# Kernel tuning notes

Hardware: AMD Instinct MI355X
Metric: run time of the kernel (lower is better)

## Reference

```python
import jax, jax.numpy as jnp
import numpy as np

N, E, H, NF, MN, ME = 4096, 65536, 128, 4, 8, 4
DEPTH, RATIO, NT = 5, 0.2, 2


def _k_list():
    ks, n = [], N
    for _ in range(DEPTH):
        n = int(np.ceil(RATIO * n))
        ks.append(n)
    return ks

K_LIST = _k_list()  # [820, 164, 33, 7, 2]


def _gcn(A, x, W, b, fill):
    # GCNConv on dense adjacency: D^-1/2 (A + fill*I) D^-1/2 @ (x W) + b
    n = A.shape[0]
    Ah = A + fill * jnp.eye(n, dtype=A.dtype)
    deg = jnp.sum(Ah, axis=1)
    dinv = jnp.where(deg > 0, jax.lax.rsqrt(jnp.maximum(deg, 1e-12)), 0.0)
    return (dinv[:, None] * Ah * dinv[None, :]) @ (x @ W) + b


def _augment(A):
    # GraphUNet.augment_adj: remove self loops, add weight-1 loops, A@A, remove self loops
    n = A.shape[0]
    eye = jnp.eye(n, dtype=A.dtype)
    A1 = A * (1.0 - eye) + eye
    A2 = A1 @ A1
    return A2 * (1.0 - eye)


def _topk_pool(A, x, w, k):
    # TopKPooling: score = tanh(x.w / ||w||), keep top-k, scale kept features by score
    score = jnp.tanh((x @ w) / jnp.linalg.norm(w))
    sv, perm = jax.lax.top_k(score, k)
    return x[perm] * sv[:, None], A[perm][:, perm], perm


def _graph_unet(A0, x, Wd0, bd0, Wd, bd, pool_w, Wu, bu):
    act = jax.nn.relu
    x = act(_gcn(A0, x, Wd0, bd0, 2.0))  # improved GCN: fill=2
    xs, As, perms = [x], [A0], []
    A = A0
    for i in range(DEPTH):
        A = _augment(A)
        x, A, perm = _topk_pool(A, x, pool_w[i], K_LIST[i])
        x = act(_gcn(A, x, Wd[i], bd[i], 2.0))
        if i < DEPTH - 1:
            xs.append(x)
            As.append(A)
        perms.append(perm)
    for i in range(DEPTH):
        j = DEPTH - 1 - i
        res, Aj, perm = xs[j], As[j], perms[j]
        up = jnp.zeros_like(res).at[perm].set(x)
        x = _gcn(Aj, res + up, Wu[i], bu[i], 2.0)  # sum_res=True
        if i < DEPTH - 1:
            x = act(x)
    return x


def _forward(F_0, mesh_node, mesh_edge, Wm, bm, Wd0, bd0, Wd, bd, pool_w,
             Wu, bu, Wout, bout, edge_index, n_time):
    src, dst = edge_index[0], edge_index[1]
    A = jnp.zeros((N, N), jnp.float32).at[dst, src].add(1.0)  # dst aggregates from src
    h = jnp.zeros((N, H), jnp.float32)
    F_cur = F_0
    Fs = []
    for _ in range(n_time):
        node_attr = jnp.concatenate([F_cur, mesh_node, h], axis=1)
        # Input: per-edge cat([x_i, x_j, e]) -> Linear -> scatter-sum by dst
        msg = jnp.concatenate([node_attr[dst], node_attr[src], mesh_edge], axis=1) @ Wm + bm
        h1 = jax.nn.relu(jax.ops.segment_sum(msg, dst, num_segments=N))
        h2 = _graph_unet(A, h1, Wd0, bd0, Wd, bd, pool_w, Wu, bu)
        h = jax.lax.stop_gradient(h2)
        h2 = jax.nn.relu(h2)
        F_next = _gcn(A, jnp.concatenate([h1, h2], axis=1), Wout, bout, 1.0)
        Fs.append(F_next)
        F_cur = jax.lax.stop_gradient(F_next)
    return jnp.stack(Fs, axis=1)  # [N, n_time, NF]


def setup_inputs() -> dict:
    key = jax.random.key(0)
    ks = jax.random.split(key, 12)
    s = 0.05
    node_in = NF + MN + H
    return {
        "F_0": jax.random.normal(ks[0], (N, NF), jnp.float32),
        "mesh_node": jax.random.normal(ks[1], (N, MN), jnp.float32),
        "mesh_edge": jax.random.normal(ks[2], (E, ME), jnp.float32),
        "Wm": jax.random.normal(ks[3], (2 * node_in + ME, H), jnp.float32) * s,
        "bm": jnp.zeros((H,), jnp.float32),
        "Wd0": jax.random.normal(ks[4], (H, H), jnp.float32) * s,
        "bd0": jnp.zeros((H,), jnp.float32),
        "Wd": jax.random.normal(ks[5], (DEPTH, H, H), jnp.float32) * s,
        "bd": jnp.zeros((DEPTH, H), jnp.float32),
        "pool_w": jax.random.normal(ks[6], (DEPTH, H), jnp.float32) * s,
        "Wu": jax.random.normal(ks[7], (DEPTH, H, H), jnp.float32) * s,
        "bu": jnp.zeros((DEPTH, H), jnp.float32),
        "Wout": jax.random.normal(ks[8], (2 * H, NF), jnp.float32) * s,
        "bout": jnp.zeros((NF,), jnp.float32),
        "edge_index": jax.random.randint(ks[9], (2, E), 0, N, dtype=jnp.int32),
        "n_time": NT,
    }


def reference(F_0, mesh_node, mesh_edge, Wm, bm, Wd0, bd0, Wd, bd, pool_w,
              Wu, bu, Wout, bout, edge_index, n_time):
    return _forward(F_0, mesh_node, mesh_edge, Wm, bm, Wd0, bd0, Wd, bd,
                    pool_w, Wu, bu, Wout, bout, edge_index, n_time)
```

## Files before the change

kernel.cpp:

```cpp
#include <hip/hip_runtime.h>
#include <math.h>

#define NN 4096
#define EE 65536
#define H 128
#define NF 4
#define MNODE 8
#define MEDGE 4
#define NT 2

__global__ void k_count(const int* __restrict__ dst, int* __restrict__ cnt) {
  int e = blockIdx.x * 256 + threadIdx.x;
  if (e < EE) atomicAdd(&cnt[dst[e]], 1);
}

__global__ void k_scan(const int* __restrict__ cnt, int* __restrict__ rp) {
  __shared__ int sh[1024];
  int t = threadIdx.x;
  int v0 = cnt[4*t], v1 = cnt[4*t+1], v2 = cnt[4*t+2], v3 = cnt[4*t+3];
  int p1 = v0, p2 = v0 + v1, p3 = p2 + v2, tot = p3 + v3;
  sh[t] = tot; __syncthreads();
  for (int off = 1; off < 1024; off <<= 1) {
    int add = (t >= off) ? sh[t-off] : 0;
    __syncthreads();
    sh[t] += add;
    __syncthreads();
  }
  int base = sh[t] - tot;
  rp[4*t] = base; rp[4*t+1] = base + p1; rp[4*t+2] = base + p2; rp[4*t+3] = base + p3;
  if (t == 1023) rp[NN] = sh[t];
}

__global__ void k_fill(const int* __restrict__ ei, int* __restrict__ cursor, int* __restrict__ cols) {
  int e = blockIdx.x * 256 + threadIdx.x;
  if (e < EE) {
    int d = ei[EE + e], s = ei[e];
    int pos = atomicAdd(&cursor[d], 1);
    cols[pos] = s;
  }
}

__global__ void k_dinv0(const int* __restrict__ cnt, float* __restrict__ d2, float* __restrict__ d1) {
  int i = blockIdx.x * 256 + threadIdx.x;
  if (i < NN) {
    float c = (float)cnt[i];
    d2[i] = 1.f / sqrtf(c + 2.f);
    d1[i] = 1.f / sqrtf(c + 1.f);
  }
}

__global__ void k_pwnorm(const float* __restrict__ pw, float* __restrict__ pwn) {
  int l = blockIdx.x, t = threadIdx.x;
  float a = pw[l*H + t], b = pw[l*H + 64 + t];
  float s = a*a + b*b;
  for (int off = 32; off > 0; off >>= 1) s += __shfl_down(s, off);
  if (t == 0) pwn[l] = sqrtf(s);
}

__global__ void k_segS(const int* __restrict__ dst, const float* __restrict__ me, float* __restrict__ S) {
  int e = blockIdx.x * 256 + threadIdx.x;
  if (e < EE) {
    int d = dst[e];
#pragma unroll
    for (int m = 0; m < MEDGE; m++) atomicAdd(&S[d*MEDGE + m], me[e*MEDGE + m]);
  }
}

__device__ __forceinline__ void score_epilogue(float v, int row, int t,
                                               const float* pw, const float* pwn1,
                                               float* scoreo, unsigned long long* keyso,
                                               int* ranko, float* r2) {
  float sp = v * pw[t];
  for (int off = 32; off > 0; off >>= 1) sp += __shfl_down(sp, off);
  if ((t & 63) == 0) r2[t >> 6] = sp;
  __syncthreads();
  if (t == 0) {
    float s = r2[0] + r2[1];
    float sc = tanhf(s / pwn1[0]);
    scoreo[row] = sc;
    float s2 = sc + 0.0f;
    unsigned u = __float_as_uint(s2);
    u ^= (unsigned)(((int)u >> 31)) | 0x80000000u;
    keyso[row] = ((unsigned long long)u << 12) | (unsigned)(4095 - row);
    ranko[row] = 0;
  }
}

__global__ void k_mm_cat(const float* __restrict__ F, const float* __restrict__ mn,
                         const float* __restrict__ h, const float* __restrict__ Wm,
                         float* __restrict__ P, float* __restrict__ Q) {
  __shared__ float as[140];
  int row = blockIdx.x, t = threadIdx.x;
  for (int c = t; c < 140; c += 128) {
    float v;
    if (c < NF) v = F[row*NF + c];
    else if (c < NF + MNODE) v = mn[row*MNODE + (c - NF)];
    else v = h[(size_t)row*H + (c - NF - MNODE)];
    as[c] = v;
  }
  __syncthreads();
  const float* BQ = Wm + 140*H;
  float ap = 0.f, aq = 0.f;
  for (int kk = 0; kk < 140; kk++) {
    float a = as[kk];
    ap += a * Wm[kk*H + t];
    aq += a * BQ[kk*H + t];
  }
  P[(size_t)row*H + t] = ap;
  Q[(size_t)row*H + t] = aq;
}

__global__ void k_spmm_h1_mm(const float* __restrict__ Q, const int* __restrict__ rp,
                             const int* __restrict__ cols, const float* __restrict__ Pm,
                             const float* __restrict__ bm, const float* __restrict__ S,
                             const float* __restrict__ WmB, const int* __restrict__ cnt,
                             const float* __restrict__ Wd0, const float* __restrict__ dinv2,
                             float* __restrict__ h1, float* __restrict__ tsb) {
  __shared__ float hs[128];
  int i = blockIdx.x, t = threadIdx.x;
  float acc = 0.f;
  int beg = rp[i], end = rp[i+1];
  for (int e = beg; e < end; e++) acc += Q[(size_t)cols[e]*H + t];
  float v = (float)cnt[i] * (Pm[(size_t)i*H + t] + bm[t]) + acc;
#pragma unroll
  for (int m = 0; m < MEDGE; m++) v += S[i*MEDGE + m] * WmB[m*H + t];
  v = fmaxf(v, 0.f);
  h1[(size_t)i*H + t] = v;
  hs[t] = v;
  __syncthreads();
  float a2 = 0.f;
  for (int kk = 0; kk < H; kk++) a2 += hs[kk] * Wd0[kk*H + t];
  tsb[(size_t)i*H + t] = a2 * dinv2[i];
}

__global__ void k_spmm_fused(const float* __restrict__ ts, const int* __restrict__ rp,
                             const int* __restrict__ cols, const float* __restrict__ dinv,
                             float fill, const float* __restrict__ bias, int relu,
                             float* __restrict__ out,
                             const float* __restrict__ pw, const float* __restrict__ pwn1,
                             float* __restrict__ scoreo, unsigned long long* __restrict__ keyso,
                             int* __restrict__ ranko) {
  __shared__ float r2[2];
  int i = blockIdx.x, t = threadIdx.x;
  float acc = 0.f;
  int beg = rp[i], end = rp[i+1];
  for (int e = beg; e < end; e++) acc += ts[(size_t)cols[e]*H + t];
  float v;
  if (dinv) {
    v = dinv[i] * (acc + fill * ts[(size_t)i*H + t]) + bias[t];
    if (relu) v = fmaxf(v, 0.f);
  } else v = acc;
  out[(size_t)i*H + t] = v;
  if (pw) score_epilogue(v, i, t, pw, pwn1, scoreo, keyso, ranko, r2);
}

__global__ void k_count_rank(const unsigned long long* __restrict__ keys, int n,
                             int* __restrict__ rank) {
  __shared__ unsigned long long sk[256];
  int t = threadIdx.x;
  int j = blockIdx.y * 256 + t;
  sk[t] = (j < n) ? keys[j] : 0ull;
  __syncthreads();
  int i = blockIdx.x * 256 + t;
  if (i >= n) return;
  unsigned long long ki = keys[i];
  int r = 0;
#pragma unroll 8
  for (int jj = 0; jj < 256; jj++) r += (sk[jj] > ki) ? 1 : 0;
  if (r) atomicAdd(&rank[i], r);
}

__global__ void k_select(const float* __restrict__ score, const int* __restrict__ rank,
                         int n, int k, int* __restrict__ perm, float* __restrict__ sv,
                         int* __restrict__ inv) {
  int i = blockIdx.x * 256 + threadIdx.x;
  if (i < n) {
    int r = rank[i];
    inv[i] = r;
    if (r < k) { perm[r] = i; sv[r] = score[i]; }
  }
}

__global__ void k_rank820(const float* __restrict__ score, const unsigned long long* __restrict__ keys,
                          int n, int k, int* __restrict__ perm, float* __restrict__ sv,
                          int* __restrict__ inv) {
  __shared__ unsigned long long ks[832];
  int t = threadIdx.x;
  for (int i = t; i < n; i += 1024) ks[i] = keys[i];
  __syncthreads();
  if (t < n) {
    unsigned long long ki = ks[t];
    int r = 0;
    for (int j = 0; j < n; j++) r += (ks[j] > ki) ? 1 : 0;
    inv[t] = r;
    if (r < k) { perm[r] = t; sv[r] = score[t]; }
  }
}

__global__ void k_mm_pool(const float* __restrict__ x, const int* __restrict__ perm,
                          const float* __restrict__ sv, const float* __restrict__ B,
                          float* __restrict__ C, const float* __restrict__ dinv) {
  __shared__ float as[128];
  int row = blockIdx.x, t = threadIdx.x;
  as[t] = x[(size_t)perm[row]*H + t] * sv[row];
  __syncthreads();
  float acc = 0.f;
  for (int kk = 0; kk < H; kk++) acc += as[kk] * B[kk*H + t];
  C[(size_t)row*H + t] = acc * dinv[row];
}

__global__ void k_mm_rb(const float* __restrict__ A, const float* __restrict__ B,
                        float* __restrict__ C, const float* __restrict__ dinv) {
  __shared__ float as[128];
  int row = blockIdx.x, t = threadIdx.x;
  as[t] = A[(size_t)row*H + t];
  __syncthreads();
  float acc = 0.f;
  for (int kk = 0; kk < H; kk++) acc += as[kk] * B[kk*H + t];
  C[(size_t)row*H + t] = acc * dinv[row];
}

__global__ void k_pool_small(const float* __restrict__ score, const unsigned long long* __restrict__ keys,
                             const float* __restrict__ x, int n, int k,
                             int* __restrict__ perm, float* __restrict__ sv,
                             int* __restrict__ inv, float* __restrict__ xp) {
  __shared__ unsigned long long ks[256];
  __shared__ int permS[40];
  __shared__ float svS[40];
  int t = threadIdx.x;
  ks[t] = (t < n) ? keys[t] : 0ull;
  __syncthreads();
  if (t < n) {
    unsigned long long ki = ks[t];
    int r = 0;
    for (int j = 0; j < n; j++) r += (ks[j] > ki) ? 1 : 0;
    inv[t] = r;
    if (r < k) {
      float sc = score[t];
      permS[r] = t; svS[r] = sc;
      perm[r] = t; sv[r] = sc;
    }
  }
  __syncthreads();
  for (int idx = t; idx < k*H; idx += 256) {
    int r = idx >> 7, c = idx & 127;
    xp[idx] = x[(size_t)permS[r]*H + c] * svS[r];
  }
}

__global__ void k_a820_f(const int* __restrict__ rp, const int* __restrict__ cols,
                         const int* __restrict__ perm, float* __restrict__ A820,
                         float* __restrict__ dv) {
  __shared__ float acc[NN];
  __shared__ float red[256];
  int r = blockIdx.x, t = threadIdx.x;
  for (int i = t; i < NN; i += 256) acc[i] = 0.f;
  __syncthreads();
  int pi = perm[r];
  int beg = rp[pi], end = rp[pi+1];
  for (int e = beg + t; e < end; e += 256) { int c = cols[e]; if (c != pi) atomicAdd(&acc[c], 1.f); }
  if (t == 0) atomicAdd(&acc[pi], 1.f);
  int wv = t >> 6, ln = t & 63;
  for (int e0 = beg + wv; e0 < end; e0 += 4) {
    int c = cols[e0];
    if (c == pi) continue;
    int b2 = rp[c], e2 = rp[c+1];
    for (int e = b2 + ln; e < e2; e += 64) { int c2 = cols[e]; if (c2 != c) atomicAdd(&acc[c2], 1.f); }
    if (ln == 0) atomicAdd(&acc[c], 1.f);
  }
  __syncthreads();
  float local = 0.f;
  for (int cc = t; cc < 820; cc += 256) {
    float val = (cc == r) ? 0.f : acc[perm[cc]];
    A820[(size_t)r*820 + cc] = val;
    local += val;
  }
  red[t] = local; __syncthreads();
  for (int off = 128; off > 0; off >>= 1) { if (t < off) red[t] += red[t+off]; __syncthreads(); }
  if (t == 0) dv[r] = 1.f / sqrtf(red[0] + 2.f);
}

__global__ void k_gathercols(const float* __restrict__ A, int n, const int* __restrict__ perm,
                             int knext, float* __restrict__ AP) {
  int idx = blockIdx.x * 256 + threadIdx.x;
  int total = n * knext;
  if (idx >= total) return;
  int kk = idx / knext, c = idx - kk * knext;
  AP[idx] = A[(size_t)kk * n + perm[c]];
}

__global__ void k_augpool2_f(const float* __restrict__ A, const float* __restrict__ AP,
                             int n, const int* __restrict__ perm, int knext,
                             float* __restrict__ out, float* __restrict__ dv) {
  __shared__ float rowb[832];
  __shared__ float red[256];
  int r = blockIdx.x, t = threadIdx.x;
  int pr = perm[r];
  for (int i = t; i < n; i += 256) rowb[i] = A[(size_t)pr*n + i];
  __syncthreads();
  float local = 0.f;
  for (int c = t; c < knext; c += 256) {
    float dot = 0.f;
#pragma unroll 8
    for (int kk = 0; kk < n; kk++) dot += rowb[kk] * AP[(size_t)kk*knext + c];
    float val = (c == r) ? 0.f : (dot + 2.f * AP[(size_t)pr*knext + c]);
    out[(size_t)r*knext + c] = val;
    local += val;
  }
  red[t] = local; __syncthreads();
  for (int off = 128; off > 0; off >>= 1) { if (t < off) red[t] += red[t+off]; __syncthreads(); }
  if (t == 0) dv[r] = 1.f / sqrtf(red[0] + 2.f);
}

__global__ void k_augpool_small(const float* __restrict__ A, int n, const int* __restrict__ perm,
                                int knext, float* __restrict__ out, float* __restrict__ dv) {
  __shared__ float rowb[256];
  __shared__ float rsum;
  int r = blockIdx.x, t = threadIdx.x;
  int pr = perm[r];
  if (t < n) rowb[t] = A[(size_t)pr*n + t];
  if (t == 0) rsum = 0.f;
  __syncthreads();
  int g = t >> 3, lane = t & 7;
  for (int c = g; c < knext; c += 32) {
    int pc = perm[c];
    float part = 0.f;
    for (int kk = lane; kk < n; kk += 8) part += rowb[kk] * A[(size_t)kk*n + pc];
    part += __shfl_down(part, 4, 8);
    part += __shfl_down(part, 2, 8);
    part += __shfl_down(part, 1, 8);
    if (lane == 0) {
      float val = (c == r) ? 0.f : (part + 2.f * rowb[pc]);
      out[(size_t)r*knext + c] = val;
      atomicAdd(&rsum, val);
    }
  }
  __syncthreads();
  if (t == 0) dv[r] = 1.f / sqrtf(rsum + 2.f);
}

__global__ void k_dense_gcn(const float* __restrict__ A, int n, const float* __restrict__ ts,
                            const float* __restrict__ dinv, float fill, const float* __restrict__ bias,
                            int relu, float* __restrict__ out,
                            const float* __restrict__ pw, const float* __restrict__ pwn1,
                            float* __restrict__ scoreo, unsigned long long* __restrict__ keyso,
                            int* __restrict__ ranko) {
  __shared__ float r2[2];
  int i = blockIdx.x, t = threadIdx.x;
  const float* Ar = A + (size_t)i * n;
  float acc = 0.f;
  int kk = 0;
  int n4 = n & ~3;
#pragma unroll 2
  for (; kk < n4; kk += 4) {
    float a0 = Ar[kk+0], a1 = Ar[kk+1], a2 = Ar[kk+2], a3 = Ar[kk+3];
    float t0 = ts[(size_t)(kk+0)*H + t];
    float t1 = ts[(size_t)(kk+1)*H + t];
    float t2 = ts[(size_t)(kk+2)*H + t];
    float t3 = ts[(size_t)(kk+3)*H + t];
    acc += a0*t0; acc += a1*t1; acc += a2*t2; acc += a3*t3;
  }
  for (; kk < n; kk++) acc += Ar[kk] * ts[(size_t)kk*H + t];
  float v = dinv[i] * (acc + fill * ts[(size_t)i*H + t]) + bias[t];
  if (relu) v = fmaxf(v, 0.f);
  out[(size_t)i*H + t] = v;
  if (pw) score_epilogue(v, i, t, pw, pwn1, scoreo, keyso, ranko, r2);
}

__global__ void k_upproj(const float* __restrict__ xs, const int* __restrict__ inv,
                         const float* __restrict__ xcur, int kk,
                         const float* __restrict__ W, const float* __restrict__ dinv,
                         float* __restrict__ tsb) {
  __shared__ float hs[128];
  int i = blockIdx.x, t = threadIdx.x;
  int r = inv[i];
  float v = xs[(size_t)i*H + t];
  if (r < kk) v += xcur[(size_t)r*H + t];
  hs[t] = v;
  __syncthreads();
  float acc = 0.f;
  for (int k2 = 0; k2 < H; k2++) acc += hs[k2] * W[k2*H + t];
  tsb[(size_t)i*H + t] = acc * dinv[i];
}

__global__ void k_outproj_r(const float* __restrict__ h1, const float* __restrict__ hbuf,
                            const float* __restrict__ Wout, const float* __restrict__ dinv1,
                            float* __restrict__ ts2) {
  int row = blockIdx.x, t = threadIdx.x;
  float p0 = 0.f, p1 = 0.f, p2 = 0.f, p3 = 0.f;
#pragma unroll
  for (int half = 0; half < 2; half++) {
    float a = h1[(size_t)row*H + half*64 + t];
    const float* w = Wout + (half*64 + t)*4;
    p0 += a*w[0]; p1 += a*w[1]; p2 += a*w[2]; p3 += a*w[3];
    float b = fmaxf(hbuf[(size_t)row*H + half*64 + t], 0.f);
    const float* w2 = Wout + (128 + half*64 + t)*4;
    p0 += b*w2[0]; p1 += b*w2[1]; p2 += b*w2[2]; p3 += b*w2[3];
  }
  for (int off = 32; off > 0; off >>= 1) {
    p0 += __shfl_down(p0, off); p1 += __shfl_down(p1, off);
    p2 += __shfl_down(p2, off); p3 += __shfl_down(p3, off);
  }
  if (t == 0) {
    float d = dinv1[row];
    ts2[row*4+0] = d*p0; ts2[row*4+1] = d*p1; ts2[row*4+2] = d*p2; ts2[row*4+3] = d*p3;
  }
}

__global__ void k_gcn_out(const float* __restrict__ ts2, const int* __restrict__ rp,
                          const int* __restrict__ cols, const float* __restrict__ dinv1,
                          const float* __restrict__ bout, float* __restrict__ Fcur,
                          float* __restrict__ dout, int tstep) {
  int i = blockIdx.x, t = threadIdx.x;
  int f = t & 3;
  float acc = 0.f;
  int beg = rp[i], end = rp[i+1];
  for (int e = beg + (t >> 2); e < end; e += 16) acc += ts2[cols[e]*4 + f];
  for (int off = 32; off >= 4; off >>= 1) acc += __shfl_down(acc, off);
  if (t < 4) {
    float v = dinv1[i] * (acc + ts2[i*4 + f]) + bout[f];
    Fcur[i*4 + f] = v;
    dout[i*(NT*NF) + tstep*NF + f] = v;
  }
}

extern "C" void kernel_launch(void* const* d_in, const int* in_sizes, int n_in,
                              void* d_out, int out_size, void* d_ws, size_t ws_size,
                              hipStream_t stream) {
  const float* F0        = (const float*)d_in[0];
  const float* mesh_node = (const float*)d_in[1];
  const float* mesh_edge = (const float*)d_in[2];
  const float* Wm        = (const float*)d_in[3];
  const float* bm        = (const float*)d_in[4];
  const float* Wd0       = (const float*)d_in[5];
  const float* bd0       = (const float*)d_in[6];
  const float* Wd        = (const float*)d_in[7];
  const float* bd        = (const float*)d_in[8];
  const float* pool_w    = (const float*)d_in[9];
  const float* Wu        = (const float*)d_in[10];
  const float* bu        = (const float*)d_in[11];
  const float* Wout      = (const float*)d_in[12];
  const float* bout      = (const float*)d_in[13];
  const int*   ei        = (const int*)d_in[14];
  float* out = (float*)d_out;

  char* p = (char*)d_ws;
  auto carve = [&](size_t bytes) -> char* {
    char* r = p;
    p += (bytes + 255) & ~(size_t)255;
    return r;
  };
  int*   cnt    = (int*)carve((size_t)NN*4);
  int*   rp     = (int*)carve((size_t)(NN+1)*4);
  int*   cursor = (int*)carve((size_t)NN*4);
  int*   cols   = (int*)carve((size_t)EE*4);
  int*   permb  = (int*)carve((size_t)5*832*4);
  float* svb    = (float*)carve((size_t)5*832*4);
  float* dinv2  = (float*)carve((size_t)NN*4);
  float* dinv1  = (float*)carve((size_t)NN*4);
  float* pwn    = (float*)carve(8*4);
  float* S      = (float*)carve((size_t)NN*MEDGE*4);
  int*   invb   = (int*)carve((size_t)5*NN*4);
  float* P      = (float*)carve((size_t)NN*H*4);
  float* Q      = (float*)carve((size_t)NN*H*4);
  float* h1     = (float*)carve((size_t)NN*H*4);
  float* hbuf   = (float*)carve((size_t)NN*H*4);
  float* tsb    = (float*)carve((size_t)NN*H*4);
  float* tmp    = (float*)carve((size_t)NN*H*4);
  float* x0     = (float*)carve((size_t)NN*H*4);
  float* x1     = (float*)carve((size_t)820*H*4);
  float* x2     = (float*)carve((size_t)164*H*4);
  float* x3     = (float*)carve((size_t)33*H*4);
  float* x4     = (float*)carve((size_t)7*H*4);
  float* xp     = (float*)carve((size_t)820*H*4);
  float* xcur   = (float*)carve((size_t)820*H*4);
  float* score  = (float*)carve((size_t)NN*4);
  unsigned long long* keysb = (unsigned long long*)carve((size_t)NN*8);
  int*   rankb  = (int*)carve((size_t)NN*4);
  float* A820   = (float*)carve((size_t)820*820*4);
  float* A164   = (float*)carve((size_t)164*164*4);
  float* A33    = (float*)carve((size_t)33*33*4);
  float* A7     = (float*)carve((size_t)7*7*4);
  float* A2b    = (float*)carve((size_t)2*2*4);
  float* dv820  = (float*)carve(820*4);
  float* dv164  = (float*)carve(164*4);
  float* dv33   = (float*)carve(33*4);
  float* dv7    = (float*)carve(7*4);
  float* dv2    = (float*)carve(2*4);
  float* ts2    = (float*)carve((size_t)NN*NF*4);
  float* Fcur   = (float*)carve((size_t)NN*NF*4);

  float* AP = tmp;

  int* perml[5]; float* svl[5]; int* invl[5];
  for (int l = 0; l < 5; l++) {
    perml[l] = permb + l*832; svl[l] = svb + l*832; invl[l] = invb + l*NN;
  }

  hipMemsetAsync(cnt, 0, (size_t)NN*4, stream);
  hipMemsetAsync(S, 0, (size_t)NN*MEDGE*4, stream);
  hipMemsetAsync(hbuf, 0, (size_t)NN*H*4, stream);
  k_count<<<EE/256, 256, 0, stream>>>(ei + EE, cnt);
  k_scan<<<1, 1024, 0, stream>>>(cnt, rp);
  hipMemcpyAsync(cursor, rp, (size_t)NN*4, hipMemcpyDeviceToDevice, stream);
  k_fill<<<EE/256, 256, 0, stream>>>(ei, cursor, cols);
  k_dinv0<<<NN/256, 256, 0, stream>>>(cnt, dinv2, dinv1);
  k_pwnorm<<<5, 64, 0, stream>>>(pool_w, pwn);
  k_segS<<<EE/256, 256, 0, stream>>>(ei + EE, mesh_edge, S);
  hipMemcpyAsync(Fcur, F0, (size_t)NN*NF*4, hipMemcpyDeviceToDevice, stream);

  for (int step = 0; step < NT; step++) {
    k_mm_cat<<<NN, 128, 0, stream>>>(Fcur, mesh_node, hbuf, Wm, P, Q);
    k_spmm_h1_mm<<<NN, 128, 0, stream>>>(Q, rp, cols, P, bm, S, Wm + 280*H, cnt,
                                         Wd0, dinv2, h1, tsb);
    k_spmm_fused<<<NN, 128, 0, stream>>>(tsb, rp, cols, dinv2, 2.f, bd0, 1, x0,
                                         pool_w, pwn, score, keysb, rankb);

    k_count_rank<<<dim3(16, 16), 256, 0, stream>>>(keysb, NN, rankb);
    k_select<<<16, 256, 0, stream>>>(score, rankb, NN, 820, perml[0], svl[0], invl[0]);
    k_a820_f<<<820, 256, 0, stream>>>(rp, cols, perml[0], A820, dv820);
    k_mm_pool<<<820, 128, 0, stream>>>(x0, perml[0], svl[0], Wd, tsb, dv820);
    k_dense_gcn<<<820, 128, 0, stream>>>(A820, 820, tsb, dv820, 2.f, bd, 1, x1,
                                         pool_w + H, pwn + 1, score, keysb, rankb);

    k_rank820<<<1, 1024, 0, stream>>>(score, keysb, 820, 164, perml[1], svl[1], invl[1]);
    k_gathercols<<<(820*164 + 255)/256, 256, 0, stream>>>(A820, 820, perml[1], 164, AP);
    k_augpool2_f<<<164, 256, 0, stream>>>(A820, AP, 820, perml[1], 164, A164, dv164);
    k_mm_pool<<<164, 128, 0, stream>>>(x1, perml[1], svl[1], Wd + 1*H*H, tsb, dv164);
    k_dense_gcn<<<164, 128, 0, stream>>>(A164, 164, tsb, dv164, 2.f, bd + 1*H, 1, x2,
                                         pool_w + 2*H, pwn + 2, score, keysb, rankb);

    k_pool_small<<<1, 256, 0, stream>>>(score, keysb, x2, 164, 33, perml[2], svl[2], invl[2], xp);
    k_augpool_small<<<33, 256, 0, stream>>>(A164, 164, perml[2], 33, A33, dv33);
    k_mm_rb<<<33, 128, 0, stream>>>(xp, Wd + 2*H*H, tsb, dv33);
    k_dense_gcn<<<33, 128, 0, stream>>>(A33, 33, tsb, dv33, 2.f, bd + 2*H, 1, x3,
                                        pool_w + 3*H, pwn + 3, score, keysb, rankb);

    k_pool_small<<<1, 256, 0, stream>>>(score, keysb, x3, 33, 7, perml[3], svl[3], invl[3], xp);
    k_augpool_small<<<7, 256, 0, stream>>>(A33, 33, perml[3], 7, A7, dv7);
    k_mm_rb<<<7, 128, 0, stream>>>(xp, Wd + 3*H*H, tsb, dv7);
    k_dense_gcn<<<7, 128, 0, stream>>>(A7, 7, tsb, dv7, 2.f, bd + 3*H, 1, x4,
                                       pool_w + 4*H, pwn + 4, score, keysb, rankb);

    k_pool_small<<<1, 256, 0, stream>>>(score, keysb, x4, 7, 2, perml[4], svl[4], invl[4], xp);
    k_augpool_small<<<2, 256, 0, stream>>>(A7, 7, perml[4], 2, A2b, dv2);
    k_mm_rb<<<2, 128, 0, stream>>>(xp, Wd + 4*H*H, tsb, dv2);
    k_dense_gcn<<<2, 128, 0, stream>>>(A2b, 2, tsb, dv2, 2.f, bd + 4*H, 1, xcur,
                                       nullptr, nullptr, nullptr, nullptr, nullptr);

    k_upproj<<<7, 128, 0, stream>>>(x4, invl[4], xcur, 2, Wu, dv7, tsb);
    k_dense_gcn<<<7, 128, 0, stream>>>(A7, 7, tsb, dv7, 2.f, bu, 1, xcur,
                                       nullptr, nullptr, nullptr, nullptr, nullptr);
    k_upproj<<<33, 128, 0, stream>>>(x3, invl[3], xcur, 7, Wu + 1*H*H, dv33, tsb);
    k_dense_gcn<<<33, 128, 0, stream>>>(A33, 33, tsb, dv33, 2.f, bu + 1*H, 1, xcur,
                                        nullptr, nullptr, nullptr, nullptr, nullptr);
    k_upproj<<<164, 128, 0, stream>>>(x2, invl[2], xcur, 33, Wu + 2*H*H, dv164, tsb);
    k_dense_gcn<<<164, 128, 0, stream>>>(A164, 164, tsb, dv164, 2.f, bu + 2*H, 1, xcur,
                                         nullptr, nullptr, nullptr, nullptr, nullptr);
    k_upproj<<<820, 128, 0, stream>>>(x1, invl[1], xcur, 164, Wu + 3*H*H, dv820, tsb);
    k_dense_gcn<<<820, 128, 0, stream>>>(A820, 820, tsb, dv820, 2.f, bu + 3*H, 1, xcur,
                                         nullptr, nullptr, nullptr, nullptr, nullptr);
    k_upproj<<<NN, 128, 0, stream>>>(x0, invl[0], xcur, 820, Wu + 4*H*H, dinv2, tsb);
    k_spmm_fused<<<NN, 128, 0, stream>>>(tsb, rp, cols, dinv2, 2.f, bu + 4*H, 0, hbuf,
                                         nullptr, nullptr, nullptr, nullptr, nullptr);

    k_outproj_r<<<NN, 64, 0, stream>>>(h1, hbuf, Wout, dinv1, ts2);
    k_gcn_out<<<NN, 64, 0, stream>>>(ts2, rp, cols, dinv1, bout, Fcur, out, step);
  }
}
```

Baseline: 764.0 us.

## Fuse deepest pooling levels and first two up-steps into one single-block kernel

```diff
diff --git a/kernel.cpp b/kernel.cpp
--- a/kernel.cpp
+++ b/kernel.cpp
@@ -381,6 +381,189 @@
   float acc = 0.f;
   for (int k2 = 0; k2 < H; k2++) acc += hs[k2] * W[k2*H + t];
   tsb[(size_t)i*H + t] = acc * dinv[i];
+}
+
+__global__ __launch_bounds__(256) void k_deep2(
+    const float* __restrict__ x3g, const float* __restrict__ A33g,
+    const float* __restrict__ dv33g, const float* __restrict__ score,
+    const unsigned long long* __restrict__ keys,
+    const float* __restrict__ pool_w, const float* __restrict__ pwn,
+    const float* __restrict__ Wd, const float* __restrict__ bd,
+    const float* __restrict__ Wu, const float* __restrict__ bu,
+    float* __restrict__ xcur) {
+  __shared__ float x3s[33*128];
+  __shared__ float xpb[33*128];
+  __shared__ float tsbb[33*128];
+  __shared__ float x4s[7*128];
+  __shared__ float xc7[7*128];
+  __shared__ float xc2[2*128];
+  __shared__ float A33s[33*33];
+  __shared__ float A7s[49];
+  __shared__ float A2s[4];
+  __shared__ float dv33s[33], dv7s[7], dv2s[2];
+  __shared__ int   perm7[7], perm2[2], inv33s[33], inv7s[7];
+  __shared__ float sv7[7], sv2[2];
+  __shared__ unsigned long long ksh[33];
+  __shared__ float scs[33];
+  int t = threadIdx.x;
+
+  for (int i = t; i < 33*128; i += 256) x3s[i] = x3g[i];
+  for (int i = t; i < 33*33; i += 256) A33s[i] = A33g[i];
+  if (t < 33) { dv33s[t] = dv33g[t]; ksh[t] = keys[t]; scs[t] = score[t]; }
+  __syncthreads();
+
+  if (t < 33) {
+    unsigned long long ki = ksh[t];
+    int r = 0;
+    for (int j = 0; j < 33; j++) r += (ksh[j] > ki) ? 1 : 0;
+    inv33s[t] = r;
+    if (r < 7) { perm7[r] = t; sv7[r] = scs[t]; }
+  }
+  __syncthreads();
+  for (int o = t; o < 7*128; o += 256) {
+    int r = o >> 7, c = o & 127;
+    xpb[o] = x3s[perm7[r]*128 + c] * sv7[r];
+  }
+  if (t < 49) {
+    int r = t / 7, c = t - 7*r;
+    int pr = perm7[r], pc = perm7[c];
+    float dot = 0.f;
+    for (int kk = 0; kk < 33; kk++) dot += A33s[pr*33 + kk] * A33s[kk*33 + pc];
+    A7s[t] = (r == c) ? 0.f : (dot + 2.f * A33s[pr*33 + pc]);
+  }
+  __syncthreads();
+  if (t < 7) {
+    float s = 0.f;
+    for (int c = 0; c < 7; c++) s += A7s[t*7 + c];
+    dv7s[t] = 1.f / sqrtf(s + 2.f);
+  }
+  __syncthreads();
+  {
+    const float* Wd3 = Wd + 3*H*H;
+    for (int o = t; o < 7*128; o += 256) {
+      int r = o >> 7, c = o & 127;
+      float acc = 0.f;
+      for (int kk = 0; kk < H; kk++) acc += xpb[r*128 + kk] * Wd3[kk*H + c];
+      tsbb[o] = acc * dv7s[r];
+    }
+  }
+  __syncthreads();
+  {
+    const float* bd3 = bd + 3*H;
+    for (int o = t; o < 7*128; o += 256) {
+      int r = o >> 7, c = o & 127;
+      float acc = 0.f;
+      for (int kk = 0; kk < 7; kk++) acc += A7s[r*7 + kk] * tsbb[kk*128 + c];
+      float v = dv7s[r] * (acc + 2.f * tsbb[o]) + bd3[c];
+      x4s[o] = fmaxf(v, 0.f);
+    }
+  }
+  __syncthreads();
+  if (t < 7) {
+    const float* pw4 = pool_w + 4*H;
+    float s = 0.f;
+    for (int c = 0; c < H; c++) s += x4s[t*128 + c] * pw4[c];
+    float sc = tanhf(s / pwn[4]);
+    scs[t] = sc;
+    float s2 = sc + 0.0f;
+    unsigned u = __float_as_uint(s2);
+    u ^= (unsigned)(((int)u >> 31)) | 0x80000000u;
+    ksh[t] = ((unsigned long long)u << 12) | (unsigned)(4095 - t);
+  }
+  __syncthreads();
+  if (t < 7) {
+    unsigned long long ki = ksh[t];
+    int r = 0;
+    for (int j = 0; j < 7; j++) r += (ksh[j] > ki) ? 1 : 0;
+    inv7s[t] = r;
+    if (r < 2) { perm2[r] = t; sv2[r] = scs[t]; }
+  }
+  __syncthreads();
+  for (int o = t; o < 2*128; o += 256) {
+    int r = o >> 7, c = o & 127;
+    xpb[o] = x4s[perm2[r]*128 + c] * sv2[r];
+  }
+  if (t < 4) {
+    int r = t >> 1, c = t & 1;
+    int pr = perm2[r], pc = perm2[c];
+    float dot = 0.f;
+    for (int kk = 0; kk < 7; kk++) dot += A7s[pr*7 + kk] * A7s[kk*7 + pc];
+    A2s[t] = (r == c) ? 0.f : (dot + 2.f * A7s[pr*7 + pc]);
+  }
+  __syncthreads();
+  if (t < 2) dv2s[t] = 1.f / sqrtf(A2s[t*2] + A2s[t*2+1] + 2.f);
+  __syncthreads();
+  {
+    const float* Wd4 = Wd + 4*H*H;
+    for (int o = t; o < 2*128; o += 256) {
+      int r = o >> 7, c = o & 127;
+      float acc = 0.f;
+      for (int kk = 0; kk < H; kk++) acc += xpb[r*128 + kk] * Wd4[kk*H + c];
+      tsbb[o] = acc * dv2s[r];
+    }
+  }
+  __syncthreads();
+  {
+    const float* bd4 = bd + 4*H;
+    for (int o = t; o < 2*128; o += 256) {
+      int r = o >> 7, c = o & 127;
+      float acc = A2s[r*2 + 0] * tsbb[c] + A2s[r*2 + 1] * tsbb[128 + c];
+      float v = dv2s[r] * (acc + 2.f * tsbb[o]) + bd4[c];
+      xc2[o] = fmaxf(v, 0.f);
+    }
+  }
+  __syncthreads();
+  for (int o = t; o < 7*128; o += 256) {
+    int r = o >> 7, c = o & 127;
+    float v = x4s[o];
+    int rr = inv7s[r];
+    if (rr < 2) v += xc2[rr*128 + c];
+    xpb[o] = v;
+  }
+  __syncthreads();
+  for (int o = t; o < 7*128; o += 256) {
+    int r = o >> 7, c = o & 127;
+    float acc = 0.f;
+    for (int kk = 0; kk < H; kk++) acc += xpb[r*128 + kk] * Wu[kk*H + c];
+    tsbb[o] = acc * dv7s[r];
+  }
+  __syncthreads();
+  for (int o = t; o < 7*128; o += 256) {
+    int r = o >> 7, c = o & 127;
+    float acc = 0.f;
+    for (int kk = 0; kk < 7; kk++) acc += A7s[r*7 + kk] * tsbb[kk*128 + c];
+    float v = dv7s[r] * (acc + 2.f * tsbb[o]) + bu[c];
+    xc7[o] = fmaxf(v, 0.f);
+  }
+  __syncthreads();
+  for (int o = t; o < 33*128; o += 256) {
+    int r = o >> 7, c = o & 127;
+    float v = x3s[o];
+    int rr = inv33s[r];
+    if (rr < 7) v += xc7[rr*128 + c];
+    xpb[o] = v;
+  }
+  __syncthreads();
+  {
+    const float* Wu1 = Wu + 1*H*H;
+    for (int o = t; o < 33*128; o += 256) {
+      int r = o >> 7, c = o & 127;
+      float acc = 0.f;
+      for (int kk = 0; kk < H; kk++) acc += xpb[r*128 + kk] * Wu1[kk*H + c];
+      tsbb[o] = acc * dv33s[r];
+    }
+  }
+  __syncthreads();
+  {
+    const float* bu1 = bu + 1*H;
+    for (int o = t; o < 33*128; o += 256) {
+      int r = o >> 7, c = o & 127;
+      float acc = 0.f;
+      for (int kk = 0; kk < 33; kk++) acc += A33s[r*33 + kk] * tsbb[kk*128 + c];
+      float v = dv33s[r] * (acc + 2.f * tsbb[o]) + bu1[c];
+      xcur[o] = fmaxf(v, 0.f);
+    }
+  }
 }
 
 __global__ void k_outproj_r(const float* __restrict__ h1, const float* __restrict__ hbuf,
@@ -491,6 +674,7 @@
   float* Fcur   = (float*)carve((size_t)NN*NF*4);
 
   float* AP = tmp;
+  (void)x4; (void)xp; (void)A7; (void)A2b; (void)dv7; (void)dv2;
 
   int* perml[5]; float* svl[5]; int* invl[5];
   for (int l = 0; l < 5; l++) {
@@ -530,30 +714,15 @@
     k_dense_gcn<<<164, 128, 0, stream>>>(A164, 164, tsb, dv164, 2.f, bd + 1*H, 1, x2,
                                          pool_w + 2*H, pwn + 2, score, keysb, rankb);
 
-    k_pool_small<<<1, 256, 0, stream>>>(score, keysb, x2, 164, 33, perml[2], svl[2], invl[2], xp);
+    k_pool_small<<<1, 256, 0, stream>>>(score, keysb, x2, 164, 33, perml[2], svl[2], invl[2], tsb);
     k_augpool_small<<<33, 256, 0, stream>>>(A164, 164, perml[2], 33, A33, dv33);
-    k_mm_rb<<<33, 128, 0, stream>>>(xp, Wd + 2*H*H, tsb, dv33);
-    k_dense_gcn<<<33, 128, 0, stream>>>(A33, 33, tsb, dv33, 2.f, bd + 2*H, 1, x3,
+    k_mm_rb<<<33, 128, 0, stream>>>(tsb, Wd + 2*H*H, tmp, dv33);
+    k_dense_gcn<<<33, 128, 0, stream>>>(A33, 33, tmp, dv33, 2.f, bd + 2*H, 1, x3,
                                         pool_w + 3*H, pwn + 3, score, keysb, rankb);
 
-    k_pool_small<<<1, 256, 0, stream>>>(score, keysb, x3, 33, 7, perml[3], svl[3], invl[3], xp);
-    k_augpool_small<<<7, 256, 0, stream>>>(A33, 33, perml[3], 7, A7, dv7);
-    k_mm_rb<<<7, 128, 0, stream>>>(xp, Wd + 3*H*H, tsb, dv7);
-    k_dense_gcn<<<7, 128, 0, stream>>>(A7, 7, tsb, dv7, 2.f, bd + 3*H, 1, x4,
-                                       pool_w + 4*H, pwn + 4, score, keysb, rankb);
-
-    k_pool_small<<<1, 256, 0, stream>>>(score, keysb, x4, 7, 2, perml[4], svl[4], invl[4], xp);
-    k_augpool_small<<<2, 256, 0, stream>>>(A7, 7, perml[4], 2, A2b, dv2);
-    k_mm_rb<<<2, 128, 0, stream>>>(xp, Wd + 4*H*H, tsb, dv2);
-    k_dense_gcn<<<2, 128, 0, stream>>>(A2b, 2, tsb, dv2, 2.f, bd + 4*H, 1, xcur,
-                                       nullptr, nullptr, nullptr, nullptr, nullptr);
-
-    k_upproj<<<7, 128, 0, stream>>>(x4, invl[4], xcur, 2, Wu, dv7, tsb);
-    k_dense_gcn<<<7, 128, 0, stream>>>(A7, 7, tsb, dv7, 2.f, bu, 1, xcur,
-                                       nullptr, nullptr, nullptr, nullptr, nullptr);
-    k_upproj<<<33, 128, 0, stream>>>(x3, invl[3], xcur, 7, Wu + 1*H*H, dv33, tsb);
-    k_dense_gcn<<<33, 128, 0, stream>>>(A33, 33, tsb, dv33, 2.f, bu + 1*H, 1, xcur,
-                                        nullptr, nullptr, nullptr, nullptr, nullptr);
+    k_deep2<<<1, 256, 0, stream>>>(x3, A33, dv33, score, keysb, pool_w, pwn,
+                                   Wd, bd, Wu, bu, xcur);
+
     k_upproj<<<164, 128, 0, stream>>>(x2, invl[2], xcur, 33, Wu + 2*H*H, dv164, tsb);
     k_dense_gcn<<<164, 128, 0, stream>>>(A164, 164, tsb, dv164, 2.f, bu + 2*H, 1, xcur,
                                          nullptr, nullptr, nullptr, nullptr, nullptr);
```

New measurement: 796.5 us. 1.04x slower.
